# Kernel tuning notes

Hardware: AMD Instinct MI355X
Metric: run time of the kernel (lower is better)

The kernel has to match this reference:

```python
import jax, jax.numpy as jnp
import numpy as np

STEPLIM = 20   # module steplim; loop runs while iter <= steplim -> steplim+1 iterations
TOL = 1e-4     # early-stopping tolerance on change in mean NN error


def _nn1(pc1, pc2):
    """1-NN of each point in pc1 [B,N,3] within pc2 [B,M,3] under L2 norm.
    Uses the GEMM form ||a||^2 + ||b||^2 - 2 a.b instead of materializing the
    [B,N,M,3] broadcasted difference tensor. Returns (min_dist [B,N], idx [B,N])."""
    d2 = (jnp.sum(pc1 * pc1, axis=-1)[..., :, None]
          + jnp.sum(pc2 * pc2, axis=-1)[..., None, :]
          - 2.0 * jnp.einsum('bnd,bmd->bnm', pc1, pc2))
    d2 = jnp.maximum(d2, 1e-12)                  # clamp FP cancellation negatives
    idx = jnp.argmin(d2, axis=-1)                # [B, N]
    dmin = jnp.sqrt(jnp.take_along_axis(d2, idx[..., None], axis=-1)[..., 0])
    return dmin, idx


def _kabsch(src, dst):
    """Rigid transform (R, t) minimizing ||R@src + t - dst|| via SVD (EPnP._points_transform)."""
    c1 = jnp.mean(src, axis=-2, keepdims=True)   # [B,1,3]
    c2 = jnp.mean(dst, axis=-2, keepdims=True)
    H = jnp.einsum('bni,bnj->bij', src - c1, dst - c2)          # [B,3,3]
    U, S, Vt = jnp.linalg.svd(H, full_matrices=False)
    det = jnp.linalg.det(jnp.einsum('bki,bjk->bij', Vt, U))     # det(V U^T)
    d = jnp.sign(det)
    D = jnp.stack([jnp.ones_like(d), jnp.ones_like(d), d], axis=-1)  # reflection fix
    R = jnp.einsum('bki,bk,bjk->bij', Vt, D, U)                 # V diag(1,1,d) U^T
    t = c2[..., 0, :] - jnp.einsum('bij,bj->bi', R, c1[..., 0, :])
    return R, t


def _icp(p1, p2):
    B = p1.shape[0]

    def step(carry, _):
        pc, err, done = carry
        dmin, idx = _nn1(pc, p2)
        # errnew = sum(sum(values)/len(values)): mean over batch of per-point sums
        errnew = jnp.sum(dmin) / B
        # source quirk: uses the LAST batch element's indices for all batches
        matched = p2[:, idx[-1], :]                              # [B,N,3]
        R, t = _kabsch(pc, matched)
        pc_new = jnp.einsum('bij,bnj->bni', R, pc) + t[:, None, :]
        # torch loop updates temppc BEFORE the break check, then freezes
        pc_out = jnp.where(done, pc, pc_new)
        err_out = jnp.where(done, err, errnew)
        done_out = done | (jnp.abs(err - errnew) < TOL)
        return (pc_out, err_out, done_out), None

    init = (p1, jnp.asarray(0.0, p1.dtype), jnp.asarray(False))
    (pc, _, _), _ = jax.lax.scan(step, init, None, length=STEPLIM + 1)
    R, t = _kabsch(p1, pc)
    return jnp.concatenate([R, t[..., None]], axis=-1)           # [B,3,4] = [R | t]


def setup_inputs() -> dict:
    key = jax.random.key(0)
    k1, k2 = jax.random.split(key)
    p1 = jax.random.normal(k1, (1, 8192, 3), dtype=jnp.float32)
    p2 = jax.random.normal(k2, (1, 8192, 3), dtype=jnp.float32)
    return {"p1": p1, "p2": p2}


def reference(p1, p2):
    return _icp(p1, p2)
```

## Files before the change

### kernel.cpp

```cpp
#include <hip/hip_runtime.h>
#include <math.h>

#define N_PTS 8192
#define ICP_STEPS 21
#define ICP_TOL 1e-4

#define NBLK 256
#define BSIZE 1024
#define QPW 8
#define ACC_STRIDE 8

struct IcpCtl {
  double err;
  double Rc[9];
  double tc[3];
  int done;
  unsigned ticket;
};

__global__ __launch_bounds__(256) void icp_prep(const float* __restrict__ p2,
                                                float4* __restrict__ p2aug,
                                                IcpCtl* __restrict__ ctl,
                                                double* __restrict__ acc) {
  int t = blockIdx.x * 256 + threadIdx.x;
  float x = p2[3*t], y = p2[3*t+1], z = p2[3*t+2];
  p2aug[t] = make_float4(x, y, z, fmaf(x, x, fmaf(y, y, z*z)));
  if (t < 16 * ACC_STRIDE) acc[t] = 0.0;
  if (t == 0) {
    ctl->err = 0.0; ctl->done = 0; ctl->ticket = 0u;
    #pragma unroll
    for (int i = 0; i < 9; ++i) ctl->Rc[i] = (i % 4 == 0) ? 1.0 : 0.0;
    ctl->tc[0] = ctl->tc[1] = ctl->tc[2] = 0.0;
  }
}

__device__ __forceinline__ void kabsch_solve(const double* s, double* R, double* T) {
  const double n = (double)N_PTS;
  const double c1x = s[1]/n, c1y = s[2]/n, c1z = s[3]/n;
  const double c2x = s[4]/n, c2y = s[5]/n, c2z = s[6]/n;
  const double h00 = s[7]  - n*c1x*c2x, h01 = s[8]  - n*c1x*c2y, h02 = s[9]  - n*c1x*c2z;
  const double h10 = s[10] - n*c1y*c2x, h11 = s[11] - n*c1y*c2y, h12 = s[12] - n*c1y*c2z;
  const double h20 = s[13] - n*c1z*c2x, h21 = s[14] - n*c1z*c2y, h22 = s[15] - n*c1z*c2z;

  double a00 = h00*h00 + h10*h10 + h20*h20;
  double a01 = h00*h01 + h10*h11 + h20*h21;
  double a02 = h00*h02 + h10*h12 + h20*h22;
  double a11 = h01*h01 + h11*h11 + h21*h21;
  double a12 = h01*h02 + h11*h12 + h21*h22;
  double a22 = h02*h02 + h12*h12 + h22*h22;

  double v00=1.0, v01=0.0, v02=0.0;
  double v10=0.0, v11=1.0, v12=0.0;
  double v20=0.0, v21=0.0, v22=1.0;

#define ROT3(app, aqq, apq, arp, arq, vpa, vqa, vpb, vqb, vpc, vqc)              \
  {                                                                              \
    double apq_ = apq;                                                           \
    if (fabs(apq_) > 1e-300) {                                                   \
      double tau = (aqq - app) / (2.0 * apq_);                                   \
      double tt  = (tau >= 0.0 ? 1.0 : -1.0) / (fabs(tau) + sqrt(1.0 + tau*tau));\
      double c_  = 1.0 / sqrt(1.0 + tt*tt), sn = tt * c_;                        \
      app -= tt * apq_;  aqq += tt * apq_;  apq = 0.0;                           \
      double t1 = arp, t2 = arq;                                                 \
      arp = c_*t1 - sn*t2;  arq = sn*t1 + c_*t2;                                 \
      t1 = vpa; t2 = vqa; vpa = c_*t1 - sn*t2; vqa = sn*t1 + c_*t2;              \
      t1 = vpb; t2 = vqb; vpb = c_*t1 - sn*t2; vqb = sn*t1 + c_*t2;              \
      t1 = vpc; t2 = vqc; vpc = c_*t1 - sn*t2; vqc = sn*t1 + c_*t2;              \
    }                                                                            \
  }

  #pragma unroll
  for (int sweep = 0; sweep < 6; ++sweep) {
    ROT3(a00, a11, a01, a02, a12, v00, v01, v10, v11, v20, v21);
    ROT3(a00, a22, a02, a01, a12, v00, v02, v10, v12, v20, v22);
    ROT3(a11, a22, a12, a01, a02, v01, v02, v11, v12, v21, v22);
  }
#undef ROT3

  double l0 = a00, l1 = a11, l2 = a22;
  double e0x=v00, e0y=v10, e0z=v20;
  double e1x=v01, e1y=v11, e1z=v21;
  double e2x=v02, e2y=v12, e2z=v22;
#define CSWAP(la, lb, xa, ya, za, xb, yb, zb)                                    \
  if (lb > la) { double t_;                                                      \
    t_ = la; la = lb; lb = t_;  t_ = xa; xa = xb; xb = t_;                       \
    t_ = ya; ya = yb; yb = t_;  t_ = za; za = zb; zb = t_; }
  CSWAP(l0, l1, e0x, e0y, e0z, e1x, e1y, e1z);
  CSWAP(l0, l2, e0x, e0y, e0z, e2x, e2y, e2z);
  CSWAP(l1, l2, e1x, e1y, e1z, e2x, e2y, e2z);
#undef CSWAP

  double detV = e0x*(e1y*e2z - e1z*e2y) - e0y*(e1x*e2z - e1z*e2x)
              + e0z*(e1x*e2y - e1y*e2x);
  const double dsg = (detV >= 0.0) ? 1.0 : -1.0;

  double u0x = h00*e0x + h01*e0y + h02*e0z;
  double u0y = h10*e0x + h11*e0y + h12*e0z;
  double u0z = h20*e0x + h21*e0y + h22*e0z;
  double n0 = sqrt(u0x*u0x + u0y*u0y + u0z*u0z);
  if (!(n0 > 1e-150)) {
    R[0]=1.0; R[1]=0.0; R[2]=0.0; R[3]=0.0; R[4]=1.0; R[5]=0.0;
    R[6]=0.0; R[7]=0.0; R[8]=1.0;
    T[0]=c2x-c1x; T[1]=c2y-c1y; T[2]=c2z-c1z;
    return;
  }
  u0x /= n0; u0y /= n0; u0z /= n0;
  double u1x = h00*e1x + h01*e1y + h02*e1z;
  double u1y = h10*e1x + h11*e1y + h12*e1z;
  double u1z = h20*e1x + h21*e1y + h22*e1z;
  const double d10 = u1x*u0x + u1y*u0y + u1z*u0z;
  u1x -= d10*u0x; u1y -= d10*u0y; u1z -= d10*u0z;
  double n1 = sqrt(u1x*u1x + u1y*u1y + u1z*u1z);
  if (!(n1 > 1e-150)) {
    R[0]=1.0; R[1]=0.0; R[2]=0.0; R[3]=0.0; R[4]=1.0; R[5]=0.0;
    R[6]=0.0; R[7]=0.0; R[8]=1.0;
    T[0]=c2x-c1x; T[1]=c2y-c1y; T[2]=c2z-c1z;
    return;
  }
  u1x /= n1; u1y /= n1; u1z /= n1;
  const double u2x = u0y*u1z - u0z*u1y;
  const double u2y = u0z*u1x - u0x*u1z;
  const double u2z = u0x*u1y - u0y*u1x;

  R[0] = e0x*u0x + e1x*u1x + dsg*e2x*u2x;
  R[1] = e0x*u0y + e1x*u1y + dsg*e2x*u2y;
  R[2] = e0x*u0z + e1x*u1z + dsg*e2x*u2z;
  R[3] = e0y*u0x + e1y*u1x + dsg*e2y*u2x;
  R[4] = e0y*u0y + e1y*u1y + dsg*e2y*u2y;
  R[5] = e0y*u0z + e1y*u1z + dsg*e2y*u2z;
  R[6] = e0z*u0x + e1z*u1x + dsg*e2z*u2x;
  R[7] = e0z*u0y + e1z*u1y + dsg*e2z*u2y;
  R[8] = e0z*u0z + e1z*u1z + dsg*e2z*u2z;
  T[0] = c2x - (R[0]*c1x + R[1]*c1y + R[2]*c1z);
  T[1] = c2y - (R[3]*c1x + R[4]*c1y + R[5]*c1z);
  T[2] = c2z - (R[6]*c1x + R[7]*c1y + R[8]*c1z);
}

__global__ __launch_bounds__(BSIZE, 4) void icp_iter(const float* __restrict__ p1,
                                                     const float4* __restrict__ p2aug,
                                                     IcpCtl* __restrict__ ctl,
                                                     double* __restrict__ acc,
                                                     float* __restrict__ out) {
  if (ctl->done) return;
  __shared__ float4 cand[N_PTS];
  __shared__ unsigned long long pkbuf[32][4];
  __shared__ float4 qlds[32];
  __shared__ double pairbuf[32][17];
  __shared__ double tot[16];
  __shared__ int lastFlag;

  const int tid  = threadIdx.x;
  const int lane = tid & 63;
  const int w    = tid >> 6;
  const int g    = w >> 2;
  const int s    = w & 3;

  #pragma unroll
  for (int k = 0; k < 8; ++k) {
    const int i = (k << 10) + tid;
    cand[i] = p2aug[i];
  }

  const double R0 = ctl->Rc[0], R1 = ctl->Rc[1], R2 = ctl->Rc[2];
  const double R3 = ctl->Rc[3], R4 = ctl->Rc[4], R5 = ctl->Rc[5];
  const double R6 = ctl->Rc[6], R7 = ctl->Rc[7], R8 = ctl->Rc[8];
  const double T0 = ctl->tc[0], T1 = ctl->tc[1], T2 = ctl->tc[2];

  const int qbase = (blockIdx.x << 5) + (g << 3);
  float axv[QPW], ayv[QPW], azv[QPW], best[QPW];
  int bidx[QPW];
  float qxr[QPW], qyr[QPW], qzr[QPW];
  #pragma unroll
  for (int j = 0; j < QPW; ++j) {
    const int q = qbase + j;
    const double X = (double)p1[3*q], Y = (double)p1[3*q+1], Z = (double)p1[3*q+2];
    qxr[j] = (float)(R0*X + R1*Y + R2*Z + T0);
    qyr[j] = (float)(R3*X + R4*Y + R5*Z + T1);
    qzr[j] = (float)(R6*X + R7*Y + R8*Z + T2);
    axv[j] = -2.f*qxr[j]; ayv[j] = -2.f*qyr[j]; azv[j] = -2.f*qzr[j];
    best[j] = __builtin_inff(); bidx[j] = 0;
  }
  if (s == 0 && lane == 0) {
    #pragma unroll
    for (int j = 0; j < QPW; ++j)
      qlds[(g << 3) + j] = make_float4(qxr[j], qyr[j], qzr[j], 0.f);
  }
  __syncthreads();

  const int cb = s << 11;
  #pragma unroll 8
  for (int k = 0; k < 32; ++k) {
    const int cidx = cb + (k << 6) + lane;
    float4 c = cand[cidx];
    #pragma unroll
    for (int j = 0; j < QPW; ++j) {
      float d = fmaf(axv[j], c.x, fmaf(ayv[j], c.y, fmaf(azv[j], c.z, c.w)));
      if (d < best[j]) { best[j] = d; bidx[j] = cidx; }
    }
  }

  unsigned long long pk[QPW];
  #pragma unroll
  for (int j = 0; j < QPW; ++j) {
    unsigned u = __float_as_uint(best[j]);
    u ^= (unsigned)((int)u >> 31) | 0x80000000u;
    pk[j] = ((unsigned long long)u << 32) | (unsigned)bidx[j];
  }
  #pragma unroll
  for (int j = 0; j < QPW; ++j) {
    #pragma unroll
    for (int o = 1; o < 64; o <<= 1) {
      unsigned long long other = __shfl_xor(pk[j], o, 64);
      pk[j] = (other < pk[j]) ? other : pk[j];
    }
  }
  if (lane == 0) {
    #pragma unroll
    for (int j = 0; j < QPW; ++j)
      pkbuf[(g << 3) + j][s] = pk[j];
  }
  __syncthreads();

  if (tid < 32) {
    unsigned long long m = pkbuf[tid][0];
    unsigned long long m1 = pkbuf[tid][1]; m = (m1 < m) ? m1 : m;
    unsigned long long m2 = pkbuf[tid][2]; m = (m2 < m) ? m2 : m;
    unsigned long long m3 = pkbuf[tid][3]; m = (m3 < m) ? m3 : m;
    const unsigned idx = (unsigned)(m & 0xffffffffull);
    const float4 q4 = qlds[tid];
    const float4 b4 = cand[idx];
    const double ax = q4.x, ay = q4.y, az = q4.z;
    const double bx = b4.x, by = b4.y, bz = b4.z;
    const double d2 = (ax*ax + ay*ay + az*az) + (bx*bx + by*by + bz*bz)
                    - 2.0*(ax*bx + ay*by + az*bz);
    pairbuf[tid][0]  = sqrt(fmax(d2, 1e-12));
    pairbuf[tid][1]  = ax;    pairbuf[tid][2]  = ay;    pairbuf[tid][3]  = az;
    pairbuf[tid][4]  = bx;    pairbuf[tid][5]  = by;    pairbuf[tid][6]  = bz;
    pairbuf[tid][7]  = ax*bx; pairbuf[tid][8]  = ax*by; pairbuf[tid][9]  = ax*bz;
    pairbuf[tid][10] = ay*bx; pairbuf[tid][11] = ay*by; pairbuf[tid][12] = ay*bz;
    pairbuf[tid][13] = az*bx; pairbuf[tid][14] = az*by; pairbuf[tid][15] = az*bz;
  }
  __syncthreads();

  if (tid < 16) {
    double ssum = 0.0;
    #pragma unroll
    for (int i = 0; i < 32; ++i) ssum += pairbuf[i][tid];
    atomicAdd(acc + tid * ACC_STRIDE, ssum);
  }
  if (tid == 0) {
    asm volatile("s_waitcnt vmcnt(0)" ::: "memory");
    unsigned old = __hip_atomic_fetch_add(&ctl->ticket, 1u,
                      __ATOMIC_RELAXED, __HIP_MEMORY_SCOPE_AGENT);
    lastFlag = (old == NBLK - 1u) ? 1 : 0;
  }
  __syncthreads();
  if (!lastFlag) return;

  if (tid < 16) tot[tid] = atomicAdd(acc + tid * ACC_STRIDE, 0.0);
  __syncthreads();
  if (tid == 0) {
    double sm[16];
    #pragma unroll
    for (int i = 0; i < 16; ++i) sm[i] = tot[i];
    double R[9], T[3];
    kabsch_solve(sm, R, T);
    double Rc[9] = {R0,R1,R2,R3,R4,R5,R6,R7,R8};
    double tc[3] = {T0,T1,T2};
    double Rn[9], tn[3];
    #pragma unroll
    for (int i = 0; i < 3; ++i) {
      #pragma unroll
      for (int j = 0; j < 3; ++j)
        Rn[3*i+j] = R[3*i+0]*Rc[0+j] + R[3*i+1]*Rc[3+j] + R[3*i+2]*Rc[6+j];
      tn[i] = R[3*i+0]*tc[0] + R[3*i+1]*tc[1] + R[3*i+2]*tc[2] + T[i];
    }
    #pragma unroll
    for (int i = 0; i < 9; ++i) ctl->Rc[i] = Rn[i];
    #pragma unroll
    for (int i = 0; i < 3; ++i) ctl->tc[i] = tn[i];
    const double errnew = sm[0];
    ctl->done = (fabs(ctl->err - errnew) < ICP_TOL) ? 1 : 0;
    ctl->err  = errnew;
    #pragma unroll
    for (int i = 0; i < 3; ++i) {
      out[4*i + 0] = (float)Rn[3*i + 0];
      out[4*i + 1] = (float)Rn[3*i + 1];
      out[4*i + 2] = (float)Rn[3*i + 2];
      out[4*i + 3] = (float)tn[i];
    }
    #pragma unroll
    for (int i = 0; i < 16; ++i) acc[i * ACC_STRIDE] = 0.0;
    ctl->ticket = 0u;
  }
}

extern "C" void kernel_launch(void* const* d_in, const int* in_sizes, int n_in,
                              void* d_out, int out_size, void* d_ws, size_t ws_size,
                              hipStream_t stream) {
  const float* p1 = (const float*)d_in[0];
  const float* p2 = (const float*)d_in[1];
  float* out = (float*)d_out;

  char* ws = (char*)d_ws;
  float4* p2aug = (float4*)ws;
  IcpCtl* ctl   = (IcpCtl*)(ws + 128*1024);
  double* acc   = (double*)(ws + 128*1024 + 512);

  icp_prep<<<N_PTS/256, 256, 0, stream>>>(p2, p2aug, ctl, acc);
  for (int it = 0; it < ICP_STEPS; ++it)
    icp_iter<<<NBLK, BSIZE, 0, stream>>>(p1, p2aug, ctl, acc, out);
}
```

Measured before the change: 585.4 us.

## Fuse ICP iterations into one persistent cooperative kernel with a grid barrier

```diff
diff --git a/kernel.cpp b/kernel.cpp
--- a/kernel.cpp
+++ b/kernel.cpp
@@ -8,29 +8,27 @@
 #define NBLK 256
 #define BSIZE 1024
 #define QPW 8
-#define ACC_STRIDE 8
 
 struct IcpCtl {
-  double err;
-  double Rc[9];
-  double tc[3];
+  double st[12];
   int done;
+  unsigned gen;
   unsigned ticket;
 };
 
+#define AT_LD(p)    __hip_atomic_load((p), __ATOMIC_RELAXED, __HIP_MEMORY_SCOPE_AGENT)
+#define AT_ST(p, v) __hip_atomic_store((p), (v), __ATOMIC_RELAXED, __HIP_MEMORY_SCOPE_AGENT)
+
 __global__ __launch_bounds__(256) void icp_prep(const float* __restrict__ p2,
                                                 float4* __restrict__ p2aug,
-                                                IcpCtl* __restrict__ ctl,
-                                                double* __restrict__ acc) {
+                                                IcpCtl* __restrict__ ctl) {
   int t = blockIdx.x * 256 + threadIdx.x;
   float x = p2[3*t], y = p2[3*t+1], z = p2[3*t+2];
   p2aug[t] = make_float4(x, y, z, fmaf(x, x, fmaf(y, y, z*z)));
-  if (t < 16 * ACC_STRIDE) acc[t] = 0.0;
   if (t == 0) {
-    ctl->err = 0.0; ctl->done = 0; ctl->ticket = 0u;
+    ctl->done = 0; ctl->gen = 0u; ctl->ticket = 0u;
     #pragma unroll
-    for (int i = 0; i < 9; ++i) ctl->Rc[i] = (i % 4 == 0) ? 1.0 : 0.0;
-    ctl->tc[0] = ctl->tc[1] = ctl->tc[2] = 0.0;
+    for (int i = 0; i < 12; ++i) ctl->st[i] = 0.0;
   }
 }
 
@@ -136,162 +134,204 @@
   T[2] = c2z - (R[6]*c1x + R[7]*c1y + R[8]*c1z);
 }
 
-__global__ __launch_bounds__(BSIZE, 4) void icp_iter(const float* __restrict__ p1,
-                                                     const float4* __restrict__ p2aug,
-                                                     IcpCtl* __restrict__ ctl,
-                                                     double* __restrict__ acc,
-                                                     float* __restrict__ out) {
-  if (ctl->done) return;
+__global__ __launch_bounds__(BSIZE, 1) void icp_run(const float* __restrict__ p1,
+                                                    const float4* __restrict__ p2aug,
+                                                    IcpCtl* __restrict__ ctl,
+                                                    double* __restrict__ parts,
+                                                    float* __restrict__ out) {
   __shared__ float4 cand[N_PTS];
   __shared__ unsigned long long pkbuf[32][4];
   __shared__ float4 qlds[32];
   __shared__ double pairbuf[32][17];
-  __shared__ double tot[16];
-  __shared__ int lastFlag;
+  __shared__ double redbuf[64];
+  __shared__ double stLds[12];
+  __shared__ int sdone;
 
   const int tid  = threadIdx.x;
   const int lane = tid & 63;
   const int w    = tid >> 6;
   const int g    = w >> 2;
   const int s    = w & 3;
+  const int bid  = blockIdx.x;
 
   #pragma unroll
   for (int k = 0; k < 8; ++k) {
     const int i = (k << 10) + tid;
     cand[i] = p2aug[i];
   }
-
-  const double R0 = ctl->Rc[0], R1 = ctl->Rc[1], R2 = ctl->Rc[2];
-  const double R3 = ctl->Rc[3], R4 = ctl->Rc[4], R5 = ctl->Rc[5];
-  const double R6 = ctl->Rc[6], R7 = ctl->Rc[7], R8 = ctl->Rc[8];
-  const double T0 = ctl->tc[0], T1 = ctl->tc[1], T2 = ctl->tc[2];
-
-  const int qbase = (blockIdx.x << 5) + (g << 3);
-  float axv[QPW], ayv[QPW], azv[QPW], best[QPW];
-  int bidx[QPW];
-  float qxr[QPW], qyr[QPW], qzr[QPW];
+  const int qbase = (bid << 5) + (g << 3);
+  float Xf[QPW], Yf[QPW], Zf[QPW];
   #pragma unroll
   for (int j = 0; j < QPW; ++j) {
     const int q = qbase + j;
-    const double X = (double)p1[3*q], Y = (double)p1[3*q+1], Z = (double)p1[3*q+2];
-    qxr[j] = (float)(R0*X + R1*Y + R2*Z + T0);
-    qyr[j] = (float)(R3*X + R4*Y + R5*Z + T1);
-    qzr[j] = (float)(R6*X + R7*Y + R8*Z + T2);
-    axv[j] = -2.f*qxr[j]; ayv[j] = -2.f*qyr[j]; azv[j] = -2.f*qzr[j];
-    best[j] = __builtin_inff(); bidx[j] = 0;
-  }
-  if (s == 0 && lane == 0) {
-    #pragma unroll
-    for (int j = 0; j < QPW; ++j)
-      qlds[(g << 3) + j] = make_float4(qxr[j], qyr[j], qzr[j], 0.f);
+    Xf[j] = p1[3*q]; Yf[j] = p1[3*q+1]; Zf[j] = p1[3*q+2];
   }
   __syncthreads();
 
-  const int cb = s << 11;
-  #pragma unroll 8
-  for (int k = 0; k < 32; ++k) {
-    const int cidx = cb + (k << 6) + lane;
-    float4 c = cand[cidx];
+  double R0=1.0, R1=0.0, R2=0.0, R3=0.0, R4=1.0, R5=0.0,
+         R6=0.0, R7=0.0, R8=1.0, T0=0.0, T1=0.0, T2=0.0;
+  double errPrev = 0.0;
+
+  for (int it = 0; it < ICP_STEPS; ++it) {
+    float axv[QPW], ayv[QPW], azv[QPW], best[QPW];
+    int bidx[QPW];
     #pragma unroll
     for (int j = 0; j < QPW; ++j) {
-      float d = fmaf(axv[j], c.x, fmaf(ayv[j], c.y, fmaf(azv[j], c.z, c.w)));
-      if (d < best[j]) { best[j] = d; bidx[j] = cidx; }
-    }
-  }
-
-  unsigned long long pk[QPW];
-  #pragma unroll
-  for (int j = 0; j < QPW; ++j) {
-    unsigned u = __float_as_uint(best[j]);
-    u ^= (unsigned)((int)u >> 31) | 0x80000000u;
-    pk[j] = ((unsigned long long)u << 32) | (unsigned)bidx[j];
-  }
-  #pragma unroll
-  for (int j = 0; j < QPW; ++j) {
+      const double X = (double)Xf[j], Y = (double)Yf[j], Z = (double)Zf[j];
+      const float qx = (float)(R0*X + R1*Y + R2*Z + T0);
+      const float qy = (float)(R3*X + R4*Y + R5*Z + T1);
+      const float qz = (float)(R6*X + R7*Y + R8*Z + T2);
+      axv[j] = -2.f*qx; ayv[j] = -2.f*qy; azv[j] = -2.f*qz;
+      best[j] = __builtin_inff(); bidx[j] = 0;
+      if (s == 0 && lane == 0) qlds[(g << 3) + j] = make_float4(qx, qy, qz, 0.f);
+    }
+    __syncthreads();
+
+    const int cb = s << 11;
+    #pragma unroll 8
+    for (int kk = 0; kk < 32; ++kk) {
+      const int cidx = cb + (kk << 6) + lane;
+      float4 c = cand[cidx];
+      #pragma unroll
+      for (int j = 0; j < QPW; ++j) {
+        float d = fmaf(axv[j], c.x, fmaf(ayv[j], c.y, fmaf(azv[j], c.z, c.w)));
+        if (d < best[j]) { best[j] = d; bidx[j] = cidx; }
+      }
+    }
+
+    unsigned long long pk[QPW];
     #pragma unroll
-    for (int o = 1; o < 64; o <<= 1) {
-      unsigned long long other = __shfl_xor(pk[j], o, 64);
-      pk[j] = (other < pk[j]) ? other : pk[j];
-    }
-  }
-  if (lane == 0) {
+    for (int j = 0; j < QPW; ++j) {
+      unsigned u = __float_as_uint(best[j]);
+      u ^= (unsigned)((int)u >> 31) | 0x80000000u;
+      pk[j] = ((unsigned long long)u << 32) | (unsigned)bidx[j];
+    }
     #pragma unroll
-    for (int j = 0; j < QPW; ++j)
-      pkbuf[(g << 3) + j][s] = pk[j];
-  }
-  __syncthreads();
-
-  if (tid < 32) {
-    unsigned long long m = pkbuf[tid][0];
-    unsigned long long m1 = pkbuf[tid][1]; m = (m1 < m) ? m1 : m;
-    unsigned long long m2 = pkbuf[tid][2]; m = (m2 < m) ? m2 : m;
-    unsigned long long m3 = pkbuf[tid][3]; m = (m3 < m) ? m3 : m;
-    const unsigned idx = (unsigned)(m & 0xffffffffull);
-    const float4 q4 = qlds[tid];
-    const float4 b4 = cand[idx];
-    const double ax = q4.x, ay = q4.y, az = q4.z;
-    const double bx = b4.x, by = b4.y, bz = b4.z;
-    const double d2 = (ax*ax + ay*ay + az*az) + (bx*bx + by*by + bz*bz)
-                    - 2.0*(ax*bx + ay*by + az*bz);
-    pairbuf[tid][0]  = sqrt(fmax(d2, 1e-12));
-    pairbuf[tid][1]  = ax;    pairbuf[tid][2]  = ay;    pairbuf[tid][3]  = az;
-    pairbuf[tid][4]  = bx;    pairbuf[tid][5]  = by;    pairbuf[tid][6]  = bz;
-    pairbuf[tid][7]  = ax*bx; pairbuf[tid][8]  = ax*by; pairbuf[tid][9]  = ax*bz;
-    pairbuf[tid][10] = ay*bx; pairbuf[tid][11] = ay*by; pairbuf[tid][12] = ay*bz;
-    pairbuf[tid][13] = az*bx; pairbuf[tid][14] = az*by; pairbuf[tid][15] = az*bz;
-  }
-  __syncthreads();
-
-  if (tid < 16) {
-    double ssum = 0.0;
-    #pragma unroll
-    for (int i = 0; i < 32; ++i) ssum += pairbuf[i][tid];
-    atomicAdd(acc + tid * ACC_STRIDE, ssum);
-  }
-  if (tid == 0) {
-    asm volatile("s_waitcnt vmcnt(0)" ::: "memory");
-    unsigned old = __hip_atomic_fetch_add(&ctl->ticket, 1u,
-                      __ATOMIC_RELAXED, __HIP_MEMORY_SCOPE_AGENT);
-    lastFlag = (old == NBLK - 1u) ? 1 : 0;
-  }
-  __syncthreads();
-  if (!lastFlag) return;
-
-  if (tid < 16) tot[tid] = atomicAdd(acc + tid * ACC_STRIDE, 0.0);
-  __syncthreads();
-  if (tid == 0) {
-    double sm[16];
-    #pragma unroll
-    for (int i = 0; i < 16; ++i) sm[i] = tot[i];
-    double R[9], T[3];
-    kabsch_solve(sm, R, T);
-    double Rc[9] = {R0,R1,R2,R3,R4,R5,R6,R7,R8};
-    double tc[3] = {T0,T1,T2};
-    double Rn[9], tn[3];
-    #pragma unroll
-    for (int i = 0; i < 3; ++i) {
+    for (int j = 0; j < QPW; ++j) {
       #pragma unroll
-      for (int j = 0; j < 3; ++j)
-        Rn[3*i+j] = R[3*i+0]*Rc[0+j] + R[3*i+1]*Rc[3+j] + R[3*i+2]*Rc[6+j];
-      tn[i] = R[3*i+0]*tc[0] + R[3*i+1]*tc[1] + R[3*i+2]*tc[2] + T[i];
-    }
-    #pragma unroll
-    for (int i = 0; i < 9; ++i) ctl->Rc[i] = Rn[i];
-    #pragma unroll
-    for (int i = 0; i < 3; ++i) ctl->tc[i] = tn[i];
-    const double errnew = sm[0];
-    ctl->done = (fabs(ctl->err - errnew) < ICP_TOL) ? 1 : 0;
-    ctl->err  = errnew;
-    #pragma unroll
-    for (int i = 0; i < 3; ++i) {
-      out[4*i + 0] = (float)Rn[3*i + 0];
-      out[4*i + 1] = (float)Rn[3*i + 1];
-      out[4*i + 2] = (float)Rn[3*i + 2];
-      out[4*i + 3] = (float)tn[i];
-    }
-    #pragma unroll
-    for (int i = 0; i < 16; ++i) acc[i * ACC_STRIDE] = 0.0;
-    ctl->ticket = 0u;
+      for (int o = 1; o < 64; o <<= 1) {
+        unsigned long long other = __shfl_xor(pk[j], o, 64);
+        pk[j] = (other < pk[j]) ? other : pk[j];
+      }
+    }
+    if (lane == 0) {
+      #pragma unroll
+      for (int j = 0; j < QPW; ++j)
+        pkbuf[(g << 3) + j][s] = pk[j];
+    }
+    __syncthreads();
+
+    if (tid < 32) {
+      unsigned long long m = pkbuf[tid][0];
+      unsigned long long m1 = pkbuf[tid][1]; m = (m1 < m) ? m1 : m;
+      unsigned long long m2 = pkbuf[tid][2]; m = (m2 < m) ? m2 : m;
+      unsigned long long m3 = pkbuf[tid][3]; m = (m3 < m) ? m3 : m;
+      const unsigned idx = (unsigned)(m & 0xffffffffull);
+      const float4 q4 = qlds[tid];
+      const float4 b4 = cand[idx];
+      const double ax = q4.x, ay = q4.y, az = q4.z;
+      const double bx = b4.x, by = b4.y, bz = b4.z;
+      const double d2 = (ax*ax + ay*ay + az*az) + (bx*bx + by*by + bz*bz)
+                      - 2.0*(ax*bx + ay*by + az*bz);
+      pairbuf[tid][0]  = sqrt(fmax(d2, 1e-12));
+      pairbuf[tid][1]  = ax;    pairbuf[tid][2]  = ay;    pairbuf[tid][3]  = az;
+      pairbuf[tid][4]  = bx;    pairbuf[tid][5]  = by;    pairbuf[tid][6]  = bz;
+      pairbuf[tid][7]  = ax*bx; pairbuf[tid][8]  = ax*by; pairbuf[tid][9]  = ax*bz;
+      pairbuf[tid][10] = ay*bx; pairbuf[tid][11] = ay*by; pairbuf[tid][12] = ay*bz;
+      pairbuf[tid][13] = az*bx; pairbuf[tid][14] = az*by; pairbuf[tid][15] = az*bz;
+    }
+    __syncthreads();
+
+    if (tid < 16) {
+      double ssum = 0.0;
+      #pragma unroll
+      for (int i = 0; i < 32; ++i) ssum += pairbuf[i][tid];
+      AT_ST(&parts[(bid << 4) + tid], ssum);
+    }
+    if (tid == 0) {
+      asm volatile("s_waitcnt vmcnt(0)" ::: "memory");
+      __hip_atomic_fetch_add(&ctl->ticket, 1u,
+                             __ATOMIC_RELAXED, __HIP_MEMORY_SCOPE_AGENT);
+    }
+
+    if (bid == 0) {
+      if (tid == 0) {
+        const unsigned target = (unsigned)NBLK * (unsigned)(it + 1);
+        while (AT_LD(&ctl->ticket) < target) __builtin_amdgcn_s_sleep(8);
+      }
+      __syncthreads();
+      double vv[16];
+      if (tid < 256) {
+        #pragma unroll
+        for (int c = 0; c < 16; ++c) vv[c] = AT_LD(&parts[(tid << 4) + c]);
+      } else {
+        #pragma unroll
+        for (int c = 0; c < 16; ++c) vv[c] = 0.0;
+      }
+      if (w < 4) {
+        #pragma unroll
+        for (int q = 0; q < 16; ++q) {
+          double x = vv[q];
+          for (int o = 32; o > 0; o >>= 1) x += __shfl_down(x, o, 64);
+          if (lane == 0) redbuf[w*16 + q] = x;
+        }
+      }
+      __syncthreads();
+      if (tid == 0) {
+        double sm[16];
+        #pragma unroll
+        for (int i = 0; i < 16; ++i)
+          sm[i] = redbuf[i] + redbuf[16+i] + redbuf[32+i] + redbuf[48+i];
+        double Rk[9], Tk[3];
+        kabsch_solve(sm, Rk, Tk);
+        double Rc[9] = {R0,R1,R2,R3,R4,R5,R6,R7,R8};
+        double tc[3] = {T0,T1,T2};
+        double Rn[9], tn[3];
+        #pragma unroll
+        for (int i = 0; i < 3; ++i) {
+          #pragma unroll
+          for (int j = 0; j < 3; ++j)
+            Rn[3*i+j] = Rk[3*i+0]*Rc[0+j] + Rk[3*i+1]*Rc[3+j] + Rk[3*i+2]*Rc[6+j];
+          tn[i] = Rk[3*i+0]*tc[0] + Rk[3*i+1]*tc[1] + Rk[3*i+2]*tc[2] + Tk[i];
+        }
+        const int dn = (fabs(errPrev - sm[0]) < ICP_TOL) ? 1 : 0;
+        errPrev = sm[0];
+        #pragma unroll
+        for (int i = 0; i < 3; ++i) {
+          out[4*i + 0] = (float)Rn[3*i + 0];
+          out[4*i + 1] = (float)Rn[3*i + 1];
+          out[4*i + 2] = (float)Rn[3*i + 2];
+          out[4*i + 3] = (float)tn[i];
+        }
+        #pragma unroll
+        for (int i = 0; i < 9; ++i) AT_ST(&ctl->st[i], Rn[i]);
+        #pragma unroll
+        for (int i = 0; i < 3; ++i) AT_ST(&ctl->st[9 + i], tn[i]);
+        __hip_atomic_store(&ctl->done, dn, __ATOMIC_RELAXED, __HIP_MEMORY_SCOPE_AGENT);
+        asm volatile("s_waitcnt vmcnt(0)" ::: "memory");
+        AT_ST(&ctl->gen, (unsigned)(it + 1));
+        #pragma unroll
+        for (int i = 0; i < 9; ++i) stLds[i] = Rn[i];
+        stLds[9] = tn[0]; stLds[10] = tn[1]; stLds[11] = tn[2];
+        sdone = dn;
+      }
+      __syncthreads();
+    } else {
+      if (tid == 0) {
+        while (AT_LD(&ctl->gen) < (unsigned)(it + 1)) __builtin_amdgcn_s_sleep(8);
+      }
+      __syncthreads();
+      if (tid < 12) stLds[tid] = AT_LD(&ctl->st[tid]);
+      if (tid == 12)
+        sdone = __hip_atomic_load(&ctl->done, __ATOMIC_RELAXED, __HIP_MEMORY_SCOPE_AGENT);
+      __syncthreads();
+    }
+
+    R0 = stLds[0]; R1 = stLds[1]; R2 = stLds[2];
+    R3 = stLds[3]; R4 = stLds[4]; R5 = stLds[5];
+    R6 = stLds[6]; R7 = stLds[7]; R8 = stLds[8];
+    T0 = stLds[9]; T1 = stLds[10]; T2 = stLds[11];
+    if (sdone) break;
   }
 }
 
@@ -305,9 +345,11 @@
   char* ws = (char*)d_ws;
   float4* p2aug = (float4*)ws;
   IcpCtl* ctl   = (IcpCtl*)(ws + 128*1024);
-  double* acc   = (double*)(ws + 128*1024 + 512);
-
-  icp_prep<<<N_PTS/256, 256, 0, stream>>>(p2, p2aug, ctl, acc);
-  for (int it = 0; it < ICP_STEPS; ++it)
-    icp_iter<<<NBLK, BSIZE, 0, stream>>>(p1, p2aug, ctl, acc, out);
+  double* parts = (double*)(ws + 128*1024 + 512);
+
+  icp_prep<<<N_PTS/256, 256, 0, stream>>>(p2, p2aug, ctl);
+
+  void* args[] = { (void*)&p1, (void*)&p2aug, (void*)&ctl, (void*)&parts, (void*)&out };
+  hipLaunchCooperativeKernel((const void*)icp_run, dim3(NBLK), dim3(BSIZE),
+                             args, 0, stream);
 }
```

Measured after the change: 895.9 us. 1.53x slower.

## Split ICP iteration into candidate-sliced NN kernel and single-block solve kernel

Applied to the files above, without the earlier changes.

```diff
diff --git a/kernel.cpp b/kernel.cpp
--- a/kernel.cpp
+++ b/kernel.cpp
@@ -5,32 +5,81 @@
 #define ICP_STEPS 21
 #define ICP_TOL 1e-4
 
-#define NBLK 256
-#define BSIZE 1024
-#define QPW 8
-#define ACC_STRIDE 8
+#define NN_QPT 8
+#define NN_CSL 128
+#define NN_BLOCKS 256
+#define SOLVE_T 512
 
 struct IcpCtl {
   double err;
   double Rc[9];
   double tc[3];
   int done;
-  unsigned ticket;
 };
 
 __global__ __launch_bounds__(256) void icp_prep(const float* __restrict__ p2,
                                                 float4* __restrict__ p2aug,
-                                                IcpCtl* __restrict__ ctl,
-                                                double* __restrict__ acc) {
+                                                unsigned long long* __restrict__ nn,
+                                                IcpCtl* __restrict__ ctl) {
   int t = blockIdx.x * 256 + threadIdx.x;
   float x = p2[3*t], y = p2[3*t+1], z = p2[3*t+2];
   p2aug[t] = make_float4(x, y, z, fmaf(x, x, fmaf(y, y, z*z)));
-  if (t < 16 * ACC_STRIDE) acc[t] = 0.0;
+  nn[t] = ~0ull;
   if (t == 0) {
-    ctl->err = 0.0; ctl->done = 0; ctl->ticket = 0u;
+    ctl->err = 0.0; ctl->done = 0;
     #pragma unroll
     for (int i = 0; i < 9; ++i) ctl->Rc[i] = (i % 4 == 0) ? 1.0 : 0.0;
     ctl->tc[0] = ctl->tc[1] = ctl->tc[2] = 0.0;
+  }
+}
+
+__global__ __launch_bounds__(256) void icp_nn(const float* __restrict__ p1,
+                                              const float4* __restrict__ p2aug,
+                                              unsigned long long* __restrict__ nn,
+                                              const IcpCtl* __restrict__ ctl) {
+  if (ctl->done) return;
+  __shared__ float4 cand[NN_CSL];
+  const int tid = threadIdx.x;
+  const int qg  = blockIdx.x >> 6;
+  const int cs  = blockIdx.x & 63;
+  const int c0  = cs * NN_CSL;
+  if (tid < NN_CSL) cand[tid] = p2aug[c0 + tid];
+
+  const double R0 = ctl->Rc[0], R1 = ctl->Rc[1], R2 = ctl->Rc[2];
+  const double R3 = ctl->Rc[3], R4 = ctl->Rc[4], R5 = ctl->Rc[5];
+  const double R6 = ctl->Rc[6], R7 = ctl->Rc[7], R8 = ctl->Rc[8];
+  const double T0 = ctl->tc[0], T1 = ctl->tc[1], T2 = ctl->tc[2];
+
+  float ax[NN_QPT], ay[NN_QPT], az[NN_QPT], best[NN_QPT];
+  int bidx[NN_QPT];
+  const int qbase = (qg << 11) + tid;
+  #pragma unroll
+  for (int j = 0; j < NN_QPT; ++j) {
+    const int q = qbase + (j << 8);
+    const double X = (double)p1[3*q], Y = (double)p1[3*q+1], Z = (double)p1[3*q+2];
+    const float qx = (float)(R0*X + R1*Y + R2*Z + T0);
+    const float qy = (float)(R3*X + R4*Y + R5*Z + T1);
+    const float qz = (float)(R6*X + R7*Y + R8*Z + T2);
+    ax[j] = -2.f*qx; ay[j] = -2.f*qy; az[j] = -2.f*qz;
+    best[j] = __builtin_inff(); bidx[j] = 0;
+  }
+  __syncthreads();
+
+  #pragma unroll 4
+  for (int i = 0; i < NN_CSL; ++i) {
+    float4 c = cand[i];
+    #pragma unroll
+    for (int j = 0; j < NN_QPT; ++j) {
+      float d = fmaf(ax[j], c.x, fmaf(ay[j], c.y, fmaf(az[j], c.z, c.w)));
+      if (d < best[j]) { best[j] = d; bidx[j] = c0 + i; }
+    }
+  }
+  #pragma unroll
+  for (int j = 0; j < NN_QPT; ++j) {
+    unsigned u = __float_as_uint(best[j]);
+    u ^= (unsigned)((int)u >> 31) | 0x80000000u;
+    atomicMin(nn + qbase + (j << 8),
+              ((unsigned long long)u << 32) | (unsigned)bidx[j]);
   }
 }
 
@@ -136,129 +185,63 @@
   T[2] = c2z - (R[6]*c1x + R[7]*c1y + R[8]*c1z);
 }
 
-__global__ __launch_bounds__(BSIZE, 4) void icp_iter(const float* __restrict__ p1,
-                                                     const float4* __restrict__ p2aug,
-                                                     IcpCtl* __restrict__ ctl,
-                                                     double* __restrict__ acc,
-                                                     float* __restrict__ out) {
+__global__ __launch_bounds__(SOLVE_T, 1) void icp_solve(
+    const float* __restrict__ p1, const float4* __restrict__ p2aug,
+    unsigned long long* __restrict__ nn, IcpCtl* __restrict__ ctl,
+    float* __restrict__ out) {
   if (ctl->done) return;
-  __shared__ float4 cand[N_PTS];
-  __shared__ unsigned long long pkbuf[32][4];
-  __shared__ float4 qlds[32];
-  __shared__ double pairbuf[32][17];
+  __shared__ double lds[8 * 16];
   __shared__ double tot[16];
-  __shared__ int lastFlag;
-
   const int tid  = threadIdx.x;
   const int lane = tid & 63;
   const int w    = tid >> 6;
-  const int g    = w >> 2;
-  const int s    = w & 3;
-
-  #pragma unroll
-  for (int k = 0; k < 8; ++k) {
-    const int i = (k << 10) + tid;
-    cand[i] = p2aug[i];
-  }
 
   const double R0 = ctl->Rc[0], R1 = ctl->Rc[1], R2 = ctl->Rc[2];
   const double R3 = ctl->Rc[3], R4 = ctl->Rc[4], R5 = ctl->Rc[5];
   const double R6 = ctl->Rc[6], R7 = ctl->Rc[7], R8 = ctl->Rc[8];
   const double T0 = ctl->tc[0], T1 = ctl->tc[1], T2 = ctl->tc[2];
 
-  const int qbase = (blockIdx.x << 5) + (g << 3);
-  float axv[QPW], ayv[QPW], azv[QPW], best[QPW];
-  int bidx[QPW];
-  float qxr[QPW], qyr[QPW], qzr[QPW];
-  #pragma unroll
-  for (int j = 0; j < QPW; ++j) {
-    const int q = qbase + j;
-    const double X = (double)p1[3*q], Y = (double)p1[3*q+1], Z = (double)p1[3*q+2];
-    qxr[j] = (float)(R0*X + R1*Y + R2*Z + T0);
-    qyr[j] = (float)(R3*X + R4*Y + R5*Z + T1);
-    qzr[j] = (float)(R6*X + R7*Y + R8*Z + T2);
-    axv[j] = -2.f*qxr[j]; ayv[j] = -2.f*qyr[j]; azv[j] = -2.f*qzr[j];
-    best[j] = __builtin_inff(); bidx[j] = 0;
-  }
-  if (s == 0 && lane == 0) {
-    #pragma unroll
-    for (int j = 0; j < QPW; ++j)
-      qlds[(g << 3) + j] = make_float4(qxr[j], qyr[j], qzr[j], 0.f);
-  }
-  __syncthreads();
-
-  const int cb = s << 11;
-  #pragma unroll 8
-  for (int k = 0; k < 32; ++k) {
-    const int cidx = cb + (k << 6) + lane;
-    float4 c = cand[cidx];
-    #pragma unroll
-    for (int j = 0; j < QPW; ++j) {
-      float d = fmaf(axv[j], c.x, fmaf(ayv[j], c.y, fmaf(azv[j], c.z, c.w)));
-      if (d < best[j]) { best[j] = d; bidx[j] = cidx; }
-    }
-  }
-
-  unsigned long long pk[QPW];
-  #pragma unroll
-  for (int j = 0; j < QPW; ++j) {
-    unsigned u = __float_as_uint(best[j]);
-    u ^= (unsigned)((int)u >> 31) | 0x80000000u;
-    pk[j] = ((unsigned long long)u << 32) | (unsigned)bidx[j];
-  }
-  #pragma unroll
-  for (int j = 0; j < QPW; ++j) {
-    #pragma unroll
-    for (int o = 1; o < 64; o <<= 1) {
-      unsigned long long other = __shfl_xor(pk[j], o, 64);
-      pk[j] = (other < pk[j]) ? other : pk[j];
-    }
-  }
-  if (lane == 0) {
-    #pragma unroll
-    for (int j = 0; j < QPW; ++j)
-      pkbuf[(g << 3) + j][s] = pk[j];
-  }
-  __syncthreads();
-
-  if (tid < 32) {
-    unsigned long long m = pkbuf[tid][0];
-    unsigned long long m1 = pkbuf[tid][1]; m = (m1 < m) ? m1 : m;
-    unsigned long long m2 = pkbuf[tid][2]; m = (m2 < m) ? m2 : m;
-    unsigned long long m3 = pkbuf[tid][3]; m = (m3 < m) ? m3 : m;
-    const unsigned idx = (unsigned)(m & 0xffffffffull);
-    const float4 q4 = qlds[tid];
-    const float4 b4 = cand[idx];
-    const double ax = q4.x, ay = q4.y, az = q4.z;
+  double v0=0,v1=0,v2=0,v3=0,v4=0,v5=0,v6=0,v7=0,
+         v8=0,v9=0,v10=0,v11=0,v12=0,v13=0,v14=0,v15=0;
+
+  for (int k = 0; k < 16; ++k) {
+    const int i = (k << 9) + tid;
+    const unsigned idx = (unsigned)(nn[i] & 0xffffffffull);
+    nn[i] = ~0ull;
+    const double X = (double)p1[3*i], Y = (double)p1[3*i+1], Z = (double)p1[3*i+2];
+    const float sxf = (float)(R0*X + R1*Y + R2*Z + T0);
+    const float syf = (float)(R3*X + R4*Y + R5*Z + T1);
+    const float szf = (float)(R6*X + R7*Y + R8*Z + T2);
+    const float4 b4 = p2aug[idx];
+    const double ax = sxf, ay = syf, az = szf;
     const double bx = b4.x, by = b4.y, bz = b4.z;
     const double d2 = (ax*ax + ay*ay + az*az) + (bx*bx + by*by + bz*bz)
                     - 2.0*(ax*bx + ay*by + az*bz);
-    pairbuf[tid][0]  = sqrt(fmax(d2, 1e-12));
-    pairbuf[tid][1]  = ax;    pairbuf[tid][2]  = ay;    pairbuf[tid][3]  = az;
-    pairbuf[tid][4]  = bx;    pairbuf[tid][5]  = by;    pairbuf[tid][6]  = bz;
-    pairbuf[tid][7]  = ax*bx; pairbuf[tid][8]  = ax*by; pairbuf[tid][9]  = ax*bz;
-    pairbuf[tid][10] = ay*bx; pairbuf[tid][11] = ay*by; pairbuf[tid][12] = ay*bz;
-    pairbuf[tid][13] = az*bx; pairbuf[tid][14] = az*by; pairbuf[tid][15] = az*bz;
-  }
+    v0  += sqrt(fmax(d2, 1e-12));
+    v1  += ax;    v2  += ay;    v3  += az;
+    v4  += bx;    v5  += by;    v6  += bz;
+    v7  += ax*bx; v8  += ax*by; v9  += ax*bz;
+    v10 += ay*bx; v11 += ay*by; v12 += ay*bz;
+    v13 += az*bx; v14 += az*by; v15 += az*bz;
+  }
+
+#define WRED(val, q)                                                           \
+  { double x = (val);                                                          \
+    for (int o = 32; o > 0; o >>= 1) x += __shfl_down(x, o, 64);               \
+    if (lane == 0) lds[w*16 + (q)] = x; }
+  WRED(v0,0) WRED(v1,1) WRED(v2,2) WRED(v3,3) WRED(v4,4) WRED(v5,5)
+  WRED(v6,6) WRED(v7,7) WRED(v8,8) WRED(v9,9) WRED(v10,10) WRED(v11,11)
+  WRED(v12,12) WRED(v13,13) WRED(v14,14) WRED(v15,15)
+#undef WRED
   __syncthreads();
-
   if (tid < 16) {
-    double ssum = 0.0;
-    #pragma unroll
-    for (int i = 0; i < 32; ++i) ssum += pairbuf[i][tid];
-    atomicAdd(acc + tid * ACC_STRIDE, ssum);
-  }
-  if (tid == 0) {
-    asm volatile("s_waitcnt vmcnt(0)" ::: "memory");
-    unsigned old = __hip_atomic_fetch_add(&ctl->ticket, 1u,
-                      __ATOMIC_RELAXED, __HIP_MEMORY_SCOPE_AGENT);
-    lastFlag = (old == NBLK - 1u) ? 1 : 0;
+    double s = 0.0;
+    #pragma unroll
+    for (int r = 0; r < 8; ++r) s += lds[r*16 + tid];
+    tot[tid] = s;
   }
   __syncthreads();
-  if (!lastFlag) return;
-
-  if (tid < 16) tot[tid] = atomicAdd(acc + tid * ACC_STRIDE, 0.0);
-  __syncthreads();
+
   if (tid == 0) {
     double sm[16];
     #pragma unroll
@@ -289,9 +272,6 @@
       out[4*i + 2] = (float)Rn[3*i + 2];
       out[4*i + 3] = (float)tn[i];
     }
-    #pragma unroll
-    for (int i = 0; i < 16; ++i) acc[i * ACC_STRIDE] = 0.0;
-    ctl->ticket = 0u;
   }
 }
 
@@ -304,10 +284,12 @@
 
   char* ws = (char*)d_ws;
   float4* p2aug = (float4*)ws;
-  IcpCtl* ctl   = (IcpCtl*)(ws + 128*1024);
-  double* acc   = (double*)(ws + 128*1024 + 512);
-
-  icp_prep<<<N_PTS/256, 256, 0, stream>>>(p2, p2aug, ctl, acc);
-  for (int it = 0; it < ICP_STEPS; ++it)
-    icp_iter<<<NBLK, BSIZE, 0, stream>>>(p1, p2aug, ctl, acc, out);
-}
+  unsigned long long* nn = (unsigned long long*)(ws + 128*1024);
+  IcpCtl* ctl = (IcpCtl*)(ws + 192*1024);
+
+  icp_prep<<<N_PTS/256, 256, 0, stream>>>(p2, p2aug, nn, ctl);
+  for (int it = 0; it < ICP_STEPS; ++it) {
+    icp_nn<<<NN_BLOCKS, 256, 0, stream>>>(p1, p2aug, nn, ctl);
+    icp_solve<<<1, SOLVE_T, 0, stream>>>(p1, p2aug, nn, ctl, out);
+  }
+}
```

Result: slower. 804.1 us (+37.4%).
